# Kernel optimization log

Hardware: AMD Instinct MI355X
Metric: run time of the kernel (lower is better)

The kernel has to match this reference:

```python
import jax, jax.numpy as jnp
import numpy as np

N = 100_000   # nodes
E = 1_600_000 # edges (avg degree 16)
F_IN = 64
H = 64


def gcn_conv(x, row, col, dinv, W, b, n):
    # PyG GCNConv: out = D^{-1/2} (A+I) D^{-1/2} (x @ W) + b
    # row/col already include self-loops; dinv = deg^{-1/2} precomputed per layer caller
    norm = dinv[row] * dinv[col]            # [E+N]
    h = x @ W                               # [N, H] small GEMM
    msg = h[row] * norm[:, None]            # [E+N, H] gather + scale
    out = jax.ops.segment_sum(msg, col, num_segments=n)  # scatter-add
    return out + b


def setup_inputs() -> dict:
    key = jax.random.key(0)
    ks = jax.random.split(key, 8)
    x = jax.random.normal(ks[0], (N, F_IN), jnp.float32)
    edge_index = jax.random.randint(ks[1], (2, E), 0, N, dtype=jnp.int32)
    s = 1.0 / np.sqrt(F_IN)
    W1 = jax.random.normal(ks[2], (F_IN, H), jnp.float32) * s
    b1 = jnp.zeros((H,), jnp.float32)
    W2 = jax.random.normal(ks[3], (H, H), jnp.float32) * s
    b2 = jnp.zeros((H,), jnp.float32)
    W3 = jax.random.normal(ks[4], (H, H), jnp.float32) * s
    b3 = jnp.zeros((H,), jnp.float32)
    return {"x": x, "edge_index": edge_index, "W1": W1, "b1": b1,
            "W2": W2, "b2": b2, "W3": W3, "b3": b3}


def reference(x, edge_index, W1, b1, W2, b2, W3, b3):
    n = x.shape[0]
    loop = jnp.arange(n, dtype=edge_index.dtype)
    row = jnp.concatenate([edge_index[0], loop])  # sources (+ self loops)
    col = jnp.concatenate([edge_index[1], loop])  # targets (+ self loops)
    deg = jax.ops.segment_sum(jnp.ones_like(col, x.dtype), col, num_segments=n)
    dinv = jnp.where(deg > 0, jax.lax.rsqrt(deg), 0.0)

    h = gcn_conv(x, row, col, dinv, W1, b1, n)
    h = jax.nn.elu(h)
    # dropout: eval mode -> identity
    h = gcn_conv(h, row, col, dinv, W2, b2, n)
    h = jax.nn.elu(h)
    h = gcn_conv(h, row, col, dinv, W3, b3, n)
    return h
```

## Files before the change

kernel.cpp:

```cpp
#include <hip/hip_runtime.h>
#include <hip/hip_bf16.h>
#include <math.h>


#define FDIM 64
#define BKT 128
#define MAXNB 1024
#define BCAP 4080

typedef float f32x2 __attribute__((ext_vector_type(2)));


__global__ __launch_bounds__(1024) void partB_kernel(const int* __restrict__ erow,
                                                     const int* __restrict__ ecol,
                                                     int* __restrict__ cursor,
                                                     int* __restrict__ extra,
                                                     unsigned* __restrict__ part,
                                                     int e, int nb, int epb) {
    __shared__ int lh[MAXNB];
    __shared__ int lbase[MAXNB];
    const int t = threadIdx.x;
    for (int i = t; i < nb; i += 1024) lh[i] = 0;
    __syncthreads();
    int s = blockIdx.x * epb;
    int en = s + epb; if (en > e) en = e;
    for (int i = s + t; i < en; i += 1024) atomicAdd(&lh[ecol[i] >> 7], 1);
    __syncthreads();
    for (int i = t; i < nb; i += 1024)
        lbase[i] = lh[i] ? atomicAdd(&cursor[i], lh[i]) : 0;
    __syncthreads();
    for (int i = t; i < nb; i += 1024) lh[i] = 0;
    __syncthreads();
    for (int i = s + t; i < en; i += 1024) {
        int c = ecol[i];
        int b = c >> 7;
        int pos = lbase[b] + atomicAdd(&lh[b], 1);
        if (pos < BCAP) part[(size_t)b * BCAP + pos] = ((unsigned)erow[i] << 7) | (unsigned)(c & 127);
        else atomicAdd(&extra[c], 1);
    }
}

__global__ __launch_bounds__(256) void adjw_kernel(const unsigned* __restrict__ part,
                                                   const int* __restrict__ cursor,
                                                   const int* __restrict__ extra,
                                                   int* __restrict__ cnt,
                                                   int* __restrict__ adjF,
                                                   int n, int cap) {
    const int b = blockIdx.x;
    const int v0 = b << 7;
    __shared__ int lc[BKT];
    const int t = threadIdx.x;
    if (t < BKT) lc[t] = 0;
    __syncthreads();
    int tot = cursor[b];
    int s1 = (tot < BCAP) ? tot : BCAP;
    const unsigned* __restrict__ pb = part + (size_t)b * BCAP;
    for (int e = t; e < s1; e += 256) {
        unsigned pk = pb[e];
        int c = pk & 127;
        int slot = atomicAdd(&lc[c], 1);
        if (slot < cap) adjF[(size_t)(v0 + c) * cap + slot] = (int)(pk >> 7);
    }
    __syncthreads();
    int nn = n - v0; if (nn > BKT) nn = BKT;
    if (t < nn) {
        int ex = extra[v0 + t];
        int d = lc[t] + ex;
        cnt[v0 + t] = (ex > 0) ? -d : d;
    }
}


__global__ __launch_bounds__(256) void gemm_kernel(const float* __restrict__ X,
                                                   const float* __restrict__ W,
                                                   const int* __restrict__ cnt,
                                                   __hip_bfloat16* __restrict__ Hout, int n) {
    __shared__ float XT[64][68];
    __shared__ float Ws[64][68];
    const int t = threadIdx.x;
    const int row0 = blockIdx.x * 64;
    #pragma unroll
    for (int i = t; i < 4096; i += 256) Ws[i >> 6][i & 63] = W[i];
    #pragma unroll
    for (int i = t; i < 4096; i += 256) {
        int r = i >> 6, c = i & 63;
        int gr = row0 + r;
        XT[c][r] = (gr < n) ? X[(size_t)gr * FDIM + c] : 0.0f;
    }
    __syncthreads();

    const int tc = t & 15;
    const int tr = t >> 4;
    float acc[4][4];
    #pragma unroll
    for (int i = 0; i < 4; i++)
        #pragma unroll
        for (int j = 0; j < 4; j++) acc[i][j] = 0.0f;

    #pragma unroll 8
    for (int k = 0; k < 64; k++) {
        float4 a = *(const float4*)&XT[k][4 * tr];
        float4 b = *(const float4*)&Ws[k][4 * tc];
        acc[0][0] += a.x * b.x; acc[0][1] += a.x * b.y; acc[0][2] += a.x * b.z; acc[0][3] += a.x * b.w;
        acc[1][0] += a.y * b.x; acc[1][1] += a.y * b.y; acc[1][2] += a.y * b.z; acc[1][3] += a.y * b.w;
        acc[2][0] += a.z * b.x; acc[2][1] += a.z * b.y; acc[2][2] += a.z * b.z; acc[2][3] += a.z * b.w;
        acc[3][0] += a.w * b.x; acc[3][1] += a.w * b.y; acc[3][2] += a.w * b.z; acc[3][3] += a.w * b.w;
    }

    #pragma unroll
    for (int i = 0; i < 4; i++) {
        int gr = row0 + 4 * tr + i;
        if (gr < n) {
            float dv = rsqrtf(fabsf((float)cnt[gr]) + 1.0f);
            union { ushort4 u; __hip_bfloat16 h[4]; } pk;
            pk.h[0] = __float2bfloat16(acc[i][0] * dv);
            pk.h[1] = __float2bfloat16(acc[i][1] * dv);
            pk.h[2] = __float2bfloat16(acc[i][2] * dv);
            pk.h[3] = __float2bfloat16(acc[i][3] * dv);
            *(ushort4*)&Hout[(size_t)gr * FDIM + 4 * tc] = pk.u;
        }
    }
}

__device__ inline f32x2 bf2f(unsigned u) {
    f32x2 r;
    r.x = __uint_as_float(u << 16);
    r.y = __uint_as_float(u & 0xffff0000u);
    return r;
}

__global__ __launch_bounds__(256) void agg_kernel(const __hip_bfloat16* __restrict__ hs,
                                                  const int* __restrict__ adjF,
                                                  const int* __restrict__ cnt,
                                                  const float* __restrict__ bias,
                                                  float* __restrict__ out,
                                                  int n, int cap, int do_elu,
                                                  const int* __restrict__ erow,
                                                  const int* __restrict__ ecol, int etot) {
    const int tid = threadIdx.x;
    const int v = blockIdx.x * 8 + (tid >> 5);
    const int lane32 = tid & 31;
    const int half = (tid >> 5) & 1;
    const bool alive = v < n;
    const unsigned* __restrict__ hsu = (const unsigned*)hs;

    int deg_raw = alive ? cnt[v] : 0;
    int deg = (deg_raw < 0) ? -deg_raw : deg_raw;
    bool slow = alive && (deg_raw < 0 || deg > cap);

    f32x2 a = (f32x2)(0.0f);
    if (alive) a = bf2f(hsu[(size_t)v * 32 + lane32]);

    if (alive && !slow) {
        const int* __restrict__ av = adjF + (size_t)v * cap;
        for (int base = 0; base < deg; base += 32) {
            int mc = deg - base; if (mc > 32) mc = 32;
            int uvec = 0;
            if (lane32 < mc) uvec = av[base + lane32];
            int g = 0;
            for (; g + 8 <= mc; g += 8) {
                int u0 = __shfl(uvec, g + 0, 32);
                int u1 = __shfl(uvec, g + 1, 32);
                int u2 = __shfl(uvec, g + 2, 32);
                int u3 = __shfl(uvec, g + 3, 32);
                int u4 = __shfl(uvec, g + 4, 32);
                int u5 = __shfl(uvec, g + 5, 32);
                int u6 = __shfl(uvec, g + 6, 32);
                int u7 = __shfl(uvec, g + 7, 32);
                unsigned w0 = hsu[(size_t)u0 * 32 + lane32];
                unsigned w1 = hsu[(size_t)u1 * 32 + lane32];
                unsigned w2 = hsu[(size_t)u2 * 32 + lane32];
                unsigned w3 = hsu[(size_t)u3 * 32 + lane32];
                unsigned w4 = hsu[(size_t)u4 * 32 + lane32];
                unsigned w5 = hsu[(size_t)u5 * 32 + lane32];
                unsigned w6 = hsu[(size_t)u6 * 32 + lane32];
                unsigned w7 = hsu[(size_t)u7 * 32 + lane32];
                a += bf2f(w0); a += bf2f(w1); a += bf2f(w2); a += bf2f(w3);
                a += bf2f(w4); a += bf2f(w5); a += bf2f(w6); a += bf2f(w7);
            }
            for (; g + 4 <= mc; g += 4) {
                int u0 = __shfl(uvec, g + 0, 32);
                int u1 = __shfl(uvec, g + 1, 32);
                int u2 = __shfl(uvec, g + 2, 32);
                int u3 = __shfl(uvec, g + 3, 32);
                unsigned w0 = hsu[(size_t)u0 * 32 + lane32];
                unsigned w1 = hsu[(size_t)u1 * 32 + lane32];
                unsigned w2 = hsu[(size_t)u2 * 32 + lane32];
                unsigned w3 = hsu[(size_t)u3 * 32 + lane32];
                a += bf2f(w0); a += bf2f(w1); a += bf2f(w2); a += bf2f(w3);
            }
            for (; g < mc; g++) {
                int u = __shfl(uvec, g, 32);
                a += bf2f(hsu[(size_t)u * 32 + lane32]);
            }
        }
    }
    if (__any(slow)) {
        for (int base = 0; base < etot; base += 32) {
            int m = etot - base; if (m > 32) m = 32;
            int c = -1, r = 0;
            if (lane32 < m) { c = ecol[base + lane32]; r = erow[base + lane32]; }
            unsigned long long b = __ballot(slow && (c == v));
            unsigned bh = (unsigned)(b >> (half * 32));
            while (bh) {
                int j = __ffs(bh) - 1;
                bh &= bh - 1;
                int u = __shfl(r, j, 32);
                if (slow) a += bf2f(hsu[(size_t)u * 32 + lane32]);
            }
        }
    }

    if (alive) {
        float dv = rsqrtf((float)deg + 1.0f);
        f32x2 bv = ((const f32x2*)bias)[lane32];
        f32x2 rr = a * dv + bv;
        float rx = rr.x, ry = rr.y;
        if (do_elu) {
            rx = (rx > 0.0f) ? rx : (__expf(rx) - 1.0f);
            ry = (ry > 0.0f) ? ry : (__expf(ry) - 1.0f);
        }
        ((float2*)out)[(size_t)v * 32 + lane32] = make_float2(rx, ry);
    }
}


extern "C" void kernel_launch(void* const* d_in, const int* in_sizes, int n_in,
                              void* d_out, int out_size, void* d_ws, size_t ws_size,
                              hipStream_t stream) {
    const float* x   = (const float*)d_in[0];
    const int*   ei  = (const int*)d_in[1];
    const float* W1  = (const float*)d_in[2];
    const float* b1  = (const float*)d_in[3];
    const float* W2  = (const float*)d_in[4];
    const float* b2  = (const float*)d_in[5];
    const float* W3  = (const float*)d_in[6];
    const float* b3  = (const float*)d_in[7];

    const int N = in_sizes[0] / FDIM;
    const int E = in_sizes[1] / 2;
    const int* erow = ei;
    const int* ecol = ei + E;

    const int NB = (N + BKT - 1) / BKT;

    char* p = (char*)d_ws;
    __hip_bfloat16* hsb = (__hip_bfloat16*)p;  p += (size_t)N * FDIM * sizeof(__hip_bfloat16);
    int*   cnt  = (int*)p;   p += (size_t)N * sizeof(int);
    int* cursor = (int*)p;   p += (size_t)(NB + 1) * sizeof(int);
    int* extra  = (int*)p;   p += (size_t)N * sizeof(int);
    int*   adjF = (int*)p;

    unsigned* part = (unsigned*)hsb;

    size_t used = (size_t)(p - (char*)d_ws);
    int cap = 64;
    while (cap > 32 && used + (size_t)N * cap * sizeof(int) > ws_size) cap -= 16;

    float* outb = (float*)d_out;

    const int TB = 256;
    const int PBLK = 256;
    const int epb = (E + PBLK - 1) / PBLK;
    const int nblkG = (N + 63) / 64;
    const int nblkA = (N + 7) / 8;

    hipMemsetAsync(cursor, 0, (size_t)(NB + 1 + N) * sizeof(int), stream);
    partB_kernel<<<PBLK, 1024, 0, stream>>>(erow, ecol, cursor, extra, part, E, NB, epb);
    adjw_kernel<<<NB, TB, 0, stream>>>(part, cursor, extra, cnt, adjF, N, cap);

    gemm_kernel<<<nblkG, TB, 0, stream>>>(x, W1, cnt, hsb, N);
    agg_kernel<<<nblkA, TB, 0, stream>>>(hsb, adjF, cnt, b1, outb, N, cap, 1, erow, ecol, E);
    gemm_kernel<<<nblkG, TB, 0, stream>>>(outb, W2, cnt, hsb, N);
    agg_kernel<<<nblkA, TB, 0, stream>>>(hsb, adjF, cnt, b2, outb, N, cap, 1, erow, ecol, E);
    gemm_kernel<<<nblkG, TB, 0, stream>>>(outb, W3, cnt, hsb, N);
    agg_kernel<<<nblkA, TB, 0, stream>>>(hsb, adjF, cnt, b3, outb, N, cap, 0, erow, ecol, E);
}
```

Before: 320.4 us.

## Fuse adjacency build with first GEMM and aggregation with next-layer GEMM

Merges the adjacency-write kernel with the layer-1 GEMM. Each aggregation+ELU is also fused with the following layer's GEMM, so the intermediate activations stay in shared memory and are never written to global memory as fp32 and re-read. This cuts the launch count from eight to five and removes two fp32 round trips per layer. In exchange, each fused block serialises eight aggregation passes before its GEMM, and it reads W directly from global/cache instead of shared. The partition buffer now gets its own workspace region instead of aliasing the bf16 buffer, which raises workspace use and may reduce cap.

```diff
diff --git a/kernel.cpp b/kernel.cpp
--- a/kernel.cpp
+++ b/kernel.cpp
@@ -10,6 +10,12 @@
 
 typedef float f32x2 __attribute__((ext_vector_type(2)));
 
+__device__ inline f32x2 bf2f(unsigned u) {
+    f32x2 r;
+    r.x = __uint_as_float(u << 16);
+    r.y = __uint_as_float(u & 0xffff0000u);
+    return r;
+}
 
 __global__ __launch_bounds__(1024) void partB_kernel(const int* __restrict__ erow,
                                                      const int* __restrict__ ecol,
@@ -40,17 +46,19 @@
     }
 }
 
-__global__ __launch_bounds__(256) void adjw_kernel(const unsigned* __restrict__ part,
-                                                   const int* __restrict__ cursor,
-                                                   const int* __restrict__ extra,
-                                                   int* __restrict__ cnt,
-                                                   int* __restrict__ adjF,
-                                                   int n, int cap) {
+__global__ __launch_bounds__(256, 4) void adjw_gemm1_kernel(
+        const unsigned* __restrict__ part, const int* __restrict__ cursor,
+        const int* __restrict__ extra, const float* __restrict__ X,
+        const float* __restrict__ W, int* __restrict__ cnt,
+        int* __restrict__ adjF, __hip_bfloat16* __restrict__ Hout,
+        int n, int cap) {
+    __shared__ int scnt[BKT];
+    __shared__ float arena[2 * 32 * 68];
     const int b = blockIdx.x;
+    const int t = threadIdx.x;
     const int v0 = b << 7;
-    __shared__ int lc[BKT];
-    const int t = threadIdx.x;
-    if (t < BKT) lc[t] = 0;
+
+    if (t < BKT) scnt[t] = 0;
     __syncthreads();
     int tot = cursor[b];
     int s1 = (tot < BCAP) ? tot : BCAP;
@@ -58,34 +66,166 @@
     for (int e = t; e < s1; e += 256) {
         unsigned pk = pb[e];
         int c = pk & 127;
-        int slot = atomicAdd(&lc[c], 1);
+        int slot = atomicAdd(&scnt[c], 1);
         if (slot < cap) adjF[(size_t)(v0 + c) * cap + slot] = (int)(pk >> 7);
     }
     __syncthreads();
-    int nn = n - v0; if (nn > BKT) nn = BKT;
+    int nn = n - v0; if (nn > BKT) nn = BKT; if (nn < 0) nn = 0;
     if (t < nn) {
         int ex = extra[v0 + t];
-        int d = lc[t] + ex;
-        cnt[v0 + t] = (ex > 0) ? -d : d;
-    }
-}
-
-
-__global__ __launch_bounds__(256) void gemm_kernel(const float* __restrict__ X,
-                                                   const float* __restrict__ W,
-                                                   const int* __restrict__ cnt,
-                                                   __hip_bfloat16* __restrict__ Hout, int n) {
-    __shared__ float XT[64][68];
-    __shared__ float Ws[64][68];
+        int d = scnt[t] + ex;
+        int sv = (ex > 0) ? -d : d;
+        cnt[v0 + t] = sv;
+        scnt[t] = sv;
+    }
+    __syncthreads();
+
+    float* XT = arena;
+    float* Ws = arena + 32 * 68;
+    const int tc = t & 15;
+    const int tr = t >> 4;
+    for (int sub = 0; sub < 2; ++sub) {
+        const int row0 = v0 + (sub << 6);
+        float acc[4][4];
+        #pragma unroll
+        for (int i = 0; i < 4; i++)
+            #pragma unroll
+            for (int j = 0; j < 4; j++) acc[i][j] = 0.0f;
+
+        #pragma unroll
+        for (int kh = 0; kh < 2; kh++) {
+            __syncthreads();
+            for (int i = t; i < 2048; i += 256) {
+                int r = i >> 6, c = i & 63;
+                Ws[r * 68 + c] = W[(kh * 32 + r) * 64 + c];
+            }
+            for (int i = t; i < 2048; i += 256) {
+                int r = i >> 5, k = i & 31;
+                int gr = row0 + r;
+                XT[k * 68 + r] = (gr < n) ? X[(size_t)gr * FDIM + kh * 32 + k] : 0.0f;
+            }
+            __syncthreads();
+            #pragma unroll 8
+            for (int k = 0; k < 32; k++) {
+                float4 a = *(const float4*)&XT[k * 68 + 4 * tr];
+                float4 bb = *(const float4*)&Ws[k * 68 + 4 * tc];
+                acc[0][0] += a.x * bb.x; acc[0][1] += a.x * bb.y; acc[0][2] += a.x * bb.z; acc[0][3] += a.x * bb.w;
+                acc[1][0] += a.y * bb.x; acc[1][1] += a.y * bb.y; acc[1][2] += a.y * bb.z; acc[1][3] += a.y * bb.w;
+                acc[2][0] += a.z * bb.x; acc[2][1] += a.z * bb.y; acc[2][2] += a.z * bb.z; acc[2][3] += a.z * bb.w;
+                acc[3][0] += a.w * bb.x; acc[3][1] += a.w * bb.y; acc[3][2] += a.w * bb.z; acc[3][3] += a.w * bb.w;
+            }
+        }
+
+        #pragma unroll
+        for (int i = 0; i < 4; i++) {
+            int gr = row0 + 4 * tr + i;
+            if (gr < n) {
+                int sc = scnt[(sub << 6) + 4 * tr + i];
+                float dv = rsqrtf(fabsf((float)sc) + 1.0f);
+                union { ushort4 u; __hip_bfloat16 h[4]; } pk;
+                pk.h[0] = __float2bfloat16(acc[i][0] * dv);
+                pk.h[1] = __float2bfloat16(acc[i][1] * dv);
+                pk.h[2] = __float2bfloat16(acc[i][2] * dv);
+                pk.h[3] = __float2bfloat16(acc[i][3] * dv);
+                *(ushort4*)&Hout[(size_t)gr * FDIM + 4 * tc] = pk.u;
+            }
+        }
+    }
+}
+
+__global__ __launch_bounds__(256, 4) void fused_kernel(
+        const __hip_bfloat16* __restrict__ hs_in, const int* __restrict__ adjF,
+        const int* __restrict__ cnt, const float* __restrict__ bias,
+        const float* __restrict__ Wn, __hip_bfloat16* __restrict__ hs_out,
+        int n, int cap, const int* __restrict__ erow,
+        const int* __restrict__ ecol, int etot) {
+    __shared__ float XT[64 * 68];
     const int t = threadIdx.x;
-    const int row0 = blockIdx.x * 64;
-    #pragma unroll
-    for (int i = t; i < 4096; i += 256) Ws[i >> 6][i & 63] = W[i];
-    #pragma unroll
-    for (int i = t; i < 4096; i += 256) {
-        int r = i >> 6, c = i & 63;
-        int gr = row0 + r;
-        XT[c][r] = (gr < n) ? X[(size_t)gr * FDIM + c] : 0.0f;
+    const int row0 = blockIdx.x << 6;
+    const int lane32 = t & 31;
+    const int half = (t >> 5) & 1;
+    const unsigned* __restrict__ hsu = (const unsigned*)hs_in;
+
+    for (int pass = 0; pass < 8; ++pass) {
+        const int c = pass * 8 + (t >> 5);
+        const int v = row0 + c;
+        const bool alive = v < n;
+        int deg_raw = alive ? cnt[v] : 0;
+        int deg = (deg_raw < 0) ? -deg_raw : deg_raw;
+        bool slow = alive && (deg_raw < 0 || deg > cap);
+
+        f32x2 a = (f32x2)(0.0f);
+        if (alive) a = bf2f(hsu[(size_t)v * 32 + lane32]);
+
+        if (alive && !slow) {
+            const int* __restrict__ av = adjF + (size_t)v * cap;
+            for (int base = 0; base < deg; base += 32) {
+                int mc = deg - base; if (mc > 32) mc = 32;
+                int uvec = 0;
+                if (lane32 < mc) uvec = av[base + lane32];
+                int g = 0;
+                for (; g + 8 <= mc; g += 8) {
+                    int u0 = __shfl(uvec, g + 0, 32);
+                    int u1 = __shfl(uvec, g + 1, 32);
+                    int u2 = __shfl(uvec, g + 2, 32);
+                    int u3 = __shfl(uvec, g + 3, 32);
+                    int u4 = __shfl(uvec, g + 4, 32);
+                    int u5 = __shfl(uvec, g + 5, 32);
+                    int u6 = __shfl(uvec, g + 6, 32);
+                    int u7 = __shfl(uvec, g + 7, 32);
+                    unsigned w0 = hsu[(size_t)u0 * 32 + lane32];
+                    unsigned w1 = hsu[(size_t)u1 * 32 + lane32];
+                    unsigned w2 = hsu[(size_t)u2 * 32 + lane32];
+                    unsigned w3 = hsu[(size_t)u3 * 32 + lane32];
+                    unsigned w4 = hsu[(size_t)u4 * 32 + lane32];
+                    unsigned w5 = hsu[(size_t)u5 * 32 + lane32];
+                    unsigned w6 = hsu[(size_t)u6 * 32 + lane32];
+                    unsigned w7 = hsu[(size_t)u7 * 32 + lane32];
+                    a += bf2f(w0); a += bf2f(w1); a += bf2f(w2); a += bf2f(w3);
+                    a += bf2f(w4); a += bf2f(w5); a += bf2f(w6); a += bf2f(w7);
+                }
+                for (; g + 4 <= mc; g += 4) {
+                    int u0 = __shfl(uvec, g + 0, 32);
+                    int u1 = __shfl(uvec, g + 1, 32);
+                    int u2 = __shfl(uvec, g + 2, 32);
+                    int u3 = __shfl(uvec, g + 3, 32);
+                    unsigned w0 = hsu[(size_t)u0 * 32 + lane32];
+                    unsigned w1 = hsu[(size_t)u1 * 32 + lane32];
+                    unsigned w2 = hsu[(size_t)u2 * 32 + lane32];
+                    unsigned w3 = hsu[(size_t)u3 * 32 + lane32];
+                    a += bf2f(w0); a += bf2f(w1); a += bf2f(w2); a += bf2f(w3);
+                }
+                for (; g < mc; g++) {
+                    int u = __shfl(uvec, g, 32);
+                    a += bf2f(hsu[(size_t)u * 32 + lane32]);
+                }
+            }
+        }
+        if (__any(slow)) {
+            for (int base = 0; base < etot; base += 32) {
+                int m = etot - base; if (m > 32) m = 32;
+                int cc = -1, r = 0;
+                if (lane32 < m) { cc = ecol[base + lane32]; r = erow[base + lane32]; }
+                unsigned long long bl = __ballot(slow && (cc == v));
+                unsigned bh = (unsigned)(bl >> (half * 32));
+                while (bh) {
+                    int j = __ffs(bh) - 1;
+                    bh &= bh - 1;
+                    int u = __shfl(r, j, 32);
+                    if (slow) a += bf2f(hsu[(size_t)u * 32 + lane32]);
+                }
+            }
+        }
+
+        float dv = rsqrtf((float)deg + 1.0f);
+        f32x2 bv = ((const f32x2*)bias)[lane32];
+        f32x2 rr = a * dv + bv;
+        float rx = rr.x, ry = rr.y;
+        rx = (rx > 0.0f) ? rx : (__expf(rx) - 1.0f);
+        ry = (ry > 0.0f) ? ry : (__expf(ry) - 1.0f);
+        if (!alive) { rx = 0.0f; ry = 0.0f; }
+        XT[(2 * lane32) * 68 + c] = rx;
+        XT[(2 * lane32 + 1) * 68 + c] = ry;
     }
     __syncthreads();
 
@@ -97,14 +237,15 @@
         #pragma unroll
         for (int j = 0; j < 4; j++) acc[i][j] = 0.0f;
 
+    const float4* __restrict__ W4 = (const float4*)Wn;
     #pragma unroll 8
     for (int k = 0; k < 64; k++) {
-        float4 a = *(const float4*)&XT[k][4 * tr];
-        float4 b = *(const float4*)&Ws[k][4 * tc];
-        acc[0][0] += a.x * b.x; acc[0][1] += a.x * b.y; acc[0][2] += a.x * b.z; acc[0][3] += a.x * b.w;
-        acc[1][0] += a.y * b.x; acc[1][1] += a.y * b.y; acc[1][2] += a.y * b.z; acc[1][3] += a.y * b.w;
-        acc[2][0] += a.z * b.x; acc[2][1] += a.z * b.y; acc[2][2] += a.z * b.z; acc[2][3] += a.z * b.w;
-        acc[3][0] += a.w * b.x; acc[3][1] += a.w * b.y; acc[3][2] += a.w * b.z; acc[3][3] += a.w * b.w;
+        float4 a = *(const float4*)&XT[k * 68 + 4 * tr];
+        float4 bb = W4[k * 16 + tc];
+        acc[0][0] += a.x * bb.x; acc[0][1] += a.x * bb.y; acc[0][2] += a.x * bb.z; acc[0][3] += a.x * bb.w;
+        acc[1][0] += a.y * bb.x; acc[1][1] += a.y * bb.y; acc[1][2] += a.y * bb.z; acc[1][3] += a.y * bb.w;
+        acc[2][0] += a.z * bb.x; acc[2][1] += a.z * bb.y; acc[2][2] += a.z * bb.z; acc[2][3] += a.z * bb.w;
+        acc[3][0] += a.w * bb.x; acc[3][1] += a.w * bb.y; acc[3][2] += a.w * bb.z; acc[3][3] += a.w * bb.w;
     }
 
     #pragma unroll
@@ -117,16 +258,9 @@
             pk.h[1] = __float2bfloat16(acc[i][1] * dv);
             pk.h[2] = __float2bfloat16(acc[i][2] * dv);
             pk.h[3] = __float2bfloat16(acc[i][3] * dv);
-            *(ushort4*)&Hout[(size_t)gr * FDIM + 4 * tc] = pk.u;
-        }
-    }
-}
-
-__device__ inline f32x2 bf2f(unsigned u) {
-    f32x2 r;
-    r.x = __uint_as_float(u << 16);
-    r.y = __uint_as_float(u & 0xffff0000u);
-    return r;
+            *(ushort4*)&hs_out[(size_t)gr * FDIM + 4 * tc] = pk.u;
+        }
+    }
 }
 
 __global__ __launch_bounds__(256) void agg_kernel(const __hip_bfloat16* __restrict__ hs,
@@ -134,7 +268,7 @@
                                                   const int* __restrict__ cnt,
                                                   const float* __restrict__ bias,
                                                   float* __restrict__ out,
-                                                  int n, int cap, int do_elu,
+                                                  int n, int cap,
                                                   const int* __restrict__ erow,
                                                   const int* __restrict__ ecol, int etot) {
     const int tid = threadIdx.x;
@@ -215,12 +349,7 @@
         float dv = rsqrtf((float)deg + 1.0f);
         f32x2 bv = ((const f32x2*)bias)[lane32];
         f32x2 rr = a * dv + bv;
-        float rx = rr.x, ry = rr.y;
-        if (do_elu) {
-            rx = (rx > 0.0f) ? rx : (__expf(rx) - 1.0f);
-            ry = (ry > 0.0f) ? ry : (__expf(ry) - 1.0f);
-        }
-        ((float2*)out)[(size_t)v * 32 + lane32] = make_float2(rx, ry);
+        ((float2*)out)[(size_t)v * 32 + lane32] = make_float2(rr.x, rr.y);
     }
 }
 
@@ -245,13 +374,13 @@
     const int NB = (N + BKT - 1) / BKT;
 
     char* p = (char*)d_ws;
-    __hip_bfloat16* hsb = (__hip_bfloat16*)p;  p += (size_t)N * FDIM * sizeof(__hip_bfloat16);
+    __hip_bfloat16* hsbA = (__hip_bfloat16*)p;  p += (size_t)N * FDIM * sizeof(__hip_bfloat16);
+    __hip_bfloat16* hsbB = (__hip_bfloat16*)p;  p += (size_t)N * FDIM * sizeof(__hip_bfloat16);
     int*   cnt  = (int*)p;   p += (size_t)N * sizeof(int);
     int* cursor = (int*)p;   p += (size_t)(NB + 1) * sizeof(int);
     int* extra  = (int*)p;   p += (size_t)N * sizeof(int);
+    unsigned* part = (unsigned*)p; p += (size_t)NB * BCAP * sizeof(unsigned);
     int*   adjF = (int*)p;
-
-    unsigned* part = (unsigned*)hsb;
 
     size_t used = (size_t)(p - (char*)d_ws);
     int cap = 64;
@@ -262,17 +391,13 @@
     const int TB = 256;
     const int PBLK = 256;
     const int epb = (E + PBLK - 1) / PBLK;
-    const int nblkG = (N + 63) / 64;
+    const int ntile = (N + 63) / 64;
     const int nblkA = (N + 7) / 8;
 
     hipMemsetAsync(cursor, 0, (size_t)(NB + 1 + N) * sizeof(int), stream);
     partB_kernel<<<PBLK, 1024, 0, stream>>>(erow, ecol, cursor, extra, part, E, NB, epb);
-    adjw_kernel<<<NB, TB, 0, stream>>>(part, cursor, extra, cnt, adjF, N, cap);
-
-    gemm_kernel<<<nblkG, TB, 0, stream>>>(x, W1, cnt, hsb, N);
-    agg_kernel<<<nblkA, TB, 0, stream>>>(hsb, adjF, cnt, b1, outb, N, cap, 1, erow, ecol, E);
-    gemm_kernel<<<nblkG, TB, 0, stream>>>(outb, W2, cnt, hsb, N);
-    agg_kernel<<<nblkA, TB, 0, stream>>>(hsb, adjF, cnt, b2, outb, N, cap, 1, erow, ecol, E);
-    gemm_kernel<<<nblkG, TB, 0, stream>>>(outb, W3, cnt, hsb, N);
-    agg_kernel<<<nblkA, TB, 0, stream>>>(hsb, adjF, cnt, b3, outb, N, cap, 0, erow, ecol, E);
-}
+    adjw_gemm1_kernel<<<NB, TB, 0, stream>>>(part, cursor, extra, x, W1, cnt, adjF, hsbA, N, cap);
+    fused_kernel<<<ntile, TB, 0, stream>>>(hsbA, adjF, cnt, b1, W2, hsbB, N, cap, erow, ecol, E);
+    fused_kernel<<<ntile, TB, 0, stream>>>(hsbB, adjF, cnt, b2, W3, hsbA, N, cap, erow, ecol, E);
+    agg_kernel<<<nblkA, TB, 0, stream>>>(hsbA, adjF, cnt, b3, outb, N, cap, erow, ecol, E);
+}
```

Result: faster. 295.4 us (-7.8%).
